# Performance work log

Measured on AMD Instinct MI355X. Metric: run time of the kernel, lower is better.

Reference implementation:

```python
import jax, jax.numpy as jnp
import numpy as np

T, N, F, H, L, E = 8, 50000, 64, 32, 64, 800000


def setup_inputs() -> dict:
    key = jax.random.key(0)
    ks = jax.random.split(key, 10)
    return {
        "x_seq": jax.random.normal(ks[0], (T, N, F), jnp.float32),
        "edge_index": jax.random.randint(ks[1], (T, 2, E), 0, N, jnp.int32),
        "conv_w": jax.random.normal(ks[2], (F, H), jnp.float32) * 0.1,
        "conv_b": jax.random.normal(ks[3], (H,), jnp.float32) * 0.1,
        "w_ih": jax.random.normal(ks[4], (4 * L, H), jnp.float32) * 0.1,
        "w_hh": jax.random.normal(ks[5], (4 * L, L), jnp.float32) * 0.1,
        "b_ih": jax.random.normal(ks[6], (4 * L,), jnp.float32) * 0.1,
        "b_hh": jax.random.normal(ks[7], (4 * L,), jnp.float32) * 0.1,
        "fc_w": jax.random.normal(ks[8], (1, L), jnp.float32) * 0.1,
        "fc_b": jax.random.normal(ks[9], (1,), jnp.float32) * 0.1,
    }


def reference(x_seq, edge_index, conv_w, conv_b, w_ih, w_hh, b_ih, b_hh, fc_w, fc_b):
    n = x_seq.shape[1]

    def gcn(x, ei):
        # GCNConv: add self loops, symmetric D^-1/2 (A+I) D^-1/2 normalization
        loop = jnp.arange(n, dtype=ei.dtype)
        src = jnp.concatenate([ei[0], loop])
        dst = jnp.concatenate([ei[1], loop])
        deg = jax.ops.segment_sum(jnp.ones_like(src, dtype=x.dtype), dst, num_segments=n)
        dinv = jnp.where(deg > 0, jax.lax.rsqrt(deg), 0.0)
        xw = x @ conv_w                              # [N,H]
        norm = dinv[src] * dinv[dst]                 # [E+N]
        msg = norm[:, None] * xw[src]                # [E+N,H]
        return jax.ops.segment_sum(msg, dst, num_segments=n) + conv_b

    h = jax.vmap(gcn)(x_seq, edge_index)             # [T,N,H]
    seq = jax.nn.relu(h).mean(axis=1)                # [T,H] mean-pool over nodes

    # single-layer LSTM, batch=1, torch gate order i,f,g,o
    l = w_hh.shape[1]

    def step(carry, xt):
        hp, cp = carry
        gates = xt @ w_ih.T + b_ih + hp @ w_hh.T + b_hh
        i, f, g, o = jnp.split(gates, 4)
        i, f, o = jax.nn.sigmoid(i), jax.nn.sigmoid(f), jax.nn.sigmoid(o)
        g = jnp.tanh(g)
        c = f * cp + i * g
        hn = o * jnp.tanh(c)
        return (hn, c), hn

    init = (jnp.zeros((l,), x_seq.dtype), jnp.zeros((l,), x_seq.dtype))
    (h_last, _), _ = jax.lax.scan(step, init, seq)
    out = h_last @ fc_w[0] + fc_b[0]                 # scalar (squeezed)
    return out
```

## Files before the change

kernel.cpp:

```cpp
#include <hip/hip_runtime.h>
#include <hip/hip_bf16.h>
#include <cstdint>
#include <cstddef>

#define T_DIM 8
#define N_NODES 50000
#define F_DIM 64
#define H_DIM 32
#define L_DIM 64
#define E_EDGES 800000

#define NB 128
#define NPB 391
#define BIN_CAP 8192
#define CHUNK_A 4000
#define DF_CAP 7400
#define NBLK_G2 782

typedef __attribute__((ext_vector_type(8))) short short8;
typedef __attribute__((ext_vector_type(4))) float f32x4;

__device__ __forceinline__ unsigned short f2bf(float f) {
  unsigned u = __float_as_uint(f);
  u = u + 0x7FFFu + ((u >> 16) & 1u);
  return (unsigned short)(u >> 16);
}
__device__ __forceinline__ float bf2f(unsigned short b) {
  return __uint_as_float(((unsigned)b) << 16);
}
__device__ __forceinline__ void addbf8(float* a, uint4 u) {
  a[0] += __uint_as_float(u.x << 16);
  a[1] += __uint_as_float(u.x & 0xFFFF0000u);
  a[2] += __uint_as_float(u.y << 16);
  a[3] += __uint_as_float(u.y & 0xFFFF0000u);
  a[4] += __uint_as_float(u.z << 16);
  a[5] += __uint_as_float(u.z & 0xFFFF0000u);
  a[6] += __uint_as_float(u.w << 16);
  a[7] += __uint_as_float(u.w & 0xFFFF0000u);
}
__device__ __forceinline__ short8 pack8(float4 lo, float4 hi) {
  short8 r;
  r[0] = (short)f2bf(lo.x); r[1] = (short)f2bf(lo.y);
  r[2] = (short)f2bf(lo.z); r[3] = (short)f2bf(lo.w);
  r[4] = (short)f2bf(hi.x); r[5] = (short)f2bf(hi.y);
  r[6] = (short)f2bf(hi.z); r[7] = (short)f2bf(hi.w);
  return r;
}

__global__ void k_part(const int* __restrict__ ei, int* __restrict__ bincur,
                       int* __restrict__ binbuf) {
  int t = blockIdx.x & 7;
  int e0 = (blockIdx.x >> 3) * CHUNK_A;
  const int4* d4 = reinterpret_cast<const int4*>(ei + (size_t)(t * 2 + 1) * E_EDGES + e0);
  const int4* s4 = reinterpret_cast<const int4*>(ei + (size_t)(t * 2 + 0) * E_EDGES + e0);
  __shared__ int hist[NB], bbase[NB], loff[NB], cur[NB];
  __shared__ unsigned sorted[CHUNK_A];
  __shared__ unsigned short dstb[CHUNK_A];
  __shared__ int wtot_sh;
  int tid = threadIdx.x;
  if (tid < NB) hist[tid] = 0;
  __syncthreads();
  for (int q = tid; q < CHUNK_A / 4; q += 256) {
    int4 d = d4[q];
    ushort4 pk;
    pk.x = (unsigned short)d.x; pk.y = (unsigned short)d.y;
    pk.z = (unsigned short)d.z; pk.w = (unsigned short)d.w;
    *reinterpret_cast<ushort4*>(&dstb[4 * q]) = pk;
    #pragma unroll
    for (int k = 0; k < 4; ++k) {
      int dst = (k == 0) ? d.x : (k == 1) ? d.y : (k == 2) ? d.z : d.w;
      atomicAdd(&hist[dst / NPB], 1);
    }
  }
  __syncthreads();
  int lane = tid & 63;
  int v = (tid < NB) ? hist[tid] : 0;
  int sc = v;
  #pragma unroll
  for (int o = 1; o < 64; o <<= 1) {
    int xx = __shfl_up(sc, o, 64);
    if (lane >= o) sc += xx;
  }
  if (tid == 63) wtot_sh = sc;
  __syncthreads();
  if (tid < NB) {
    int excl = sc - v + ((tid >= 64) ? wtot_sh : 0);
    loff[tid] = excl;
    cur[tid] = excl;
    bbase[tid] = atomicAdd(&bincur[t * NB + tid], v);
  }
  __syncthreads();
  for (int q = tid; q < CHUNK_A / 4; q += 256) {
    int4 s = s4[q];
    ushort4 dd = *reinterpret_cast<const ushort4*>(&dstb[4 * q]);
    #pragma unroll
    for (int k = 0; k < 4; ++k) {
      int dst = (k == 0) ? dd.x : (k == 1) ? dd.y : (k == 2) ? dd.z : dd.w;
      int src = (k == 0) ? s.x : (k == 1) ? s.y : (k == 2) ? s.z : s.w;
      int b = dst / NPB;
      int dl = dst - b * NPB;
      int pos = atomicAdd(&cur[b], 1);
      sorted[pos] = ((unsigned)b << 25) | ((unsigned)dl << 16) | (unsigned)src;
    }
  }
  __syncthreads();
  for (int i = tid; i < CHUNK_A; i += 256) {
    unsigned e = sorted[i];
    int b = e >> 25;
    int gpos = bbase[b] + (i - loff[b]);
    if (gpos < BIN_CAP)
      binbuf[(size_t)(t * NB + b) * BIN_CAP + gpos] = (int)(e & 0x01FFFFFFu);
  }
}

__global__ void k_degfill(const int* __restrict__ bincur, const int* __restrict__ binbuf,
                          int* __restrict__ deg, int* __restrict__ rowg,
                          unsigned short* __restrict__ colbuf) {
  int t = blockIdx.x & 7;
  int b = blockIdx.x >> 3;
  __shared__ int stage[DF_CAP];
  __shared__ unsigned short sbuf[DF_CAP];
  __shared__ int hist[NPB], rowoff[NPB + 1];
  __shared__ int wsum[4];
  int tid = threadIdx.x;
  int cnt = bincur[t * NB + b];
  if (cnt > DF_CAP) cnt = DF_CAP;
  const int* gbuf = binbuf + (size_t)(t * NB + b) * BIN_CAP;
  for (int i = tid; i < cnt; i += 256) stage[i] = gbuf[i];
  for (int i = tid; i < NPB; i += 256) hist[i] = 0;
  __syncthreads();
  for (int i = tid; i < cnt; i += 256) atomicAdd(&hist[stage[i] >> 16], 1);
  __syncthreads();
  int nb0 = b * NPB;
  for (int dl = tid; dl < NPB; dl += 256) {
    int n = nb0 + dl;
    if (n < N_NODES) deg[t * N_NODES + n] = hist[dl];
  }
  int i0 = 2 * tid, i1 = 2 * tid + 1;
  int a0 = (i0 < NPB) ? hist[i0] : 0;
  int a1 = (i1 < NPB) ? hist[i1] : 0;
  int tsum = a0 + a1;
  int lane = tid & 63, wid = tid >> 6;
  int sc = tsum;
  #pragma unroll
  for (int off = 1; off < 64; off <<= 1) {
    int o = __shfl_up(sc, off, 64);
    if (lane >= off) sc += o;
  }
  if (lane == 63) wsum[wid] = sc;
  __syncthreads();
  if (tid == 0) {
    int c = 0;
    for (int k = 0; k < 4; ++k) { int v = wsum[k]; wsum[k] = c; c += v; }
  }
  __syncthreads();
  int excl = wsum[wid] + (sc - tsum);
  if (i0 < NPB) rowoff[i0] = excl;
  if (i1 < NPB) rowoff[i1] = excl + a0;
  if (tid == 0) rowoff[NPB] = cnt;
  __syncthreads();
  int* rg = rowg + (size_t)(t * NB + b) * (NPB + 1);
  for (int i = tid; i <= NPB; i += 256) rg[i] = rowoff[i];
  for (int i = tid; i < NPB; i += 256) hist[i] = 0;
  __syncthreads();
  for (int i = tid; i < cnt; i += 256) {
    int w = stage[i];
    int dl = w >> 16;
    int pos = rowoff[dl] + atomicAdd(&hist[dl], 1);
    sbuf[pos] = (unsigned short)(w & 0xFFFF);
  }
  __syncthreads();
  unsigned short* cb = colbuf + (size_t)(t * NB + b) * BIN_CAP;
  for (int i = tid; i < cnt; i += 256) cb[i] = sbuf[i];
}

__global__ __launch_bounds__(256) void k_xw(const float* __restrict__ x,
                                            const float* __restrict__ w,
                                            const int* __restrict__ deg,
                                            unsigned short* __restrict__ s) {
  int t = blockIdx.x & 7;
  int nb = blockIdx.x >> 3;
  int wave = threadIdx.x >> 6, lane = threadIdx.x & 63;
  int node0 = nb * 64 + wave * 16;
  if (node0 >= N_NODES) return;
  int m = lane & 15, kg = lane >> 4;
  const float4* xr = reinterpret_cast<const float4*>(
      x + ((size_t)t * N_NODES + node0 + m) * F_DIM + kg * 8);
  short8 a0 = pack8(xr[0], xr[1]);
  short8 a1 = pack8(xr[8], xr[9]);
  const float* wb0 = w + (kg * 8) * H_DIM + m;
  const float* wb1 = wb0 + 32 * H_DIM;
  short8 b00, b01, b10, b11;
  #pragma unroll
  for (int j = 0; j < 8; ++j) {
    b00[j] = (short)f2bf(wb0[j * H_DIM]);
    b01[j] = (short)f2bf(wb0[j * H_DIM + 16]);
    b10[j] = (short)f2bf(wb1[j * H_DIM]);
    b11[j] = (short)f2bf(wb1[j * H_DIM + 16]);
  }
  f32x4 acc0 = {0.f, 0.f, 0.f, 0.f}, acc1 = {0.f, 0.f, 0.f, 0.f};
  acc0 = __builtin_amdgcn_mfma_f32_16x16x32_bf16(a0, b00, acc0, 0, 0, 0);
  acc0 = __builtin_amdgcn_mfma_f32_16x16x32_bf16(a1, b10, acc0, 0, 0, 0);
  acc1 = __builtin_amdgcn_mfma_f32_16x16x32_bf16(a0, b01, acc1, 0, 0, 0);
  acc1 = __builtin_amdgcn_mfma_f32_16x16x32_bf16(a1, b11, acc1, 0, 0, 0);
  unsigned short* sbase = s + ((size_t)t * N_NODES + node0) * H_DIM;
  #pragma unroll
  for (int r = 0; r < 4; ++r) {
    int row = kg * 4 + r;
    float dinv = rsqrtf((float)(deg[t * N_NODES + node0 + row] + 1));
    sbase[(size_t)row * H_DIM + m]      = f2bf(acc0[r] * dinv);
    sbase[(size_t)row * H_DIM + 16 + m] = f2bf(acc1[r] * dinv);
  }
}

__global__ void k_gather2(const unsigned short* __restrict__ s,
                          const unsigned short* __restrict__ colbuf,
                          const int* __restrict__ rowg, const float* __restrict__ conv_b,
                          float* __restrict__ partials) {
  int bid = blockIdx.x;
  int t = bid & 7;
  int gblk = bid >> 3;
  int tid = threadIdx.x;
  int g = tid >> 2, j = tid & 3;
  int n = gblk * 64 + g;
  float acc[8];
  #pragma unroll
  for (int e = 0; e < 8; ++e) acc[e] = 0.f;
  if (n < N_NODES) {
    int b = n / NPB, dl = n - b * NPB;
    const int* ro = rowg + (size_t)(t * NB + b) * (NPB + 1);
    int start = ro[dl], end = ro[dl + 1];
    float dinv = rsqrtf((float)(end - start + 1));
    const unsigned short* sbase = s + (size_t)t * N_NODES * H_DIM;
    uint4 su = *reinterpret_cast<const uint4*>(sbase + (size_t)n * H_DIM + j * 8);
    addbf8(acc, su);
    const unsigned short* col = colbuf + (size_t)(t * NB + b) * BIN_CAP;
    int p = start;
    for (; p + 4 <= end; p += 4) {
      int c0 = col[p], c1 = col[p + 1], c2 = col[p + 2], c3 = col[p + 3];
      uint4 v0 = *reinterpret_cast<const uint4*>(sbase + (size_t)c0 * H_DIM + j * 8);
      uint4 v1 = *reinterpret_cast<const uint4*>(sbase + (size_t)c1 * H_DIM + j * 8);
      uint4 v2 = *reinterpret_cast<const uint4*>(sbase + (size_t)c2 * H_DIM + j * 8);
      uint4 v3 = *reinterpret_cast<const uint4*>(sbase + (size_t)c3 * H_DIM + j * 8);
      addbf8(acc, v0);
      addbf8(acc, v1);
      addbf8(acc, v2);
      addbf8(acc, v3);
    }
    for (; p < end; ++p) {
      int c0 = col[p];
      uint4 v0 = *reinterpret_cast<const uint4*>(sbase + (size_t)c0 * H_DIM + j * 8);
      addbf8(acc, v0);
    }
    const float4* cb4 = reinterpret_cast<const float4*>(conv_b);
    float4 b0 = cb4[j * 2], b1 = cb4[j * 2 + 1];
    acc[0] = fmaxf(acc[0] * dinv + b0.x, 0.f);
    acc[1] = fmaxf(acc[1] * dinv + b0.y, 0.f);
    acc[2] = fmaxf(acc[2] * dinv + b0.z, 0.f);
    acc[3] = fmaxf(acc[3] * dinv + b0.w, 0.f);
    acc[4] = fmaxf(acc[4] * dinv + b1.x, 0.f);
    acc[5] = fmaxf(acc[5] * dinv + b1.y, 0.f);
    acc[6] = fmaxf(acc[6] * dinv + b1.z, 0.f);
    acc[7] = fmaxf(acc[7] * dinv + b1.w, 0.f);
  }
  #pragma unroll
  for (int off = 4; off < 64; off <<= 1) {
    #pragma unroll
    for (int e = 0; e < 8; ++e) acc[e] += __shfl_xor(acc[e], off, 64);
  }
  __shared__ float red[4][32];
  int wid = tid >> 6, lane = tid & 63;
  if (lane < 4) {
    #pragma unroll
    for (int e = 0; e < 8; ++e) red[wid][lane * 8 + e] = acc[e];
  }
  __syncthreads();
  if (tid < 32) {
    float sum = red[0][tid] + red[1][tid] + red[2][tid] + red[3][tid];
    partials[((size_t)t * NBLK_G2 + gblk) * H_DIM + tid] = sum;
  }
}

__global__ void k_reduce(const float* __restrict__ partials, float* __restrict__ seq_raw,
                         int nblk) {
  int t = blockIdx.x;
  int tid = threadIdx.x;
  int h = tid & 31, w = tid >> 5;
  float sum = 0.f;
  for (int b = w; b < nblk; b += 8) sum += partials[((size_t)t * nblk + b) * H_DIM + h];
  __shared__ float red[8][32];
  red[w][h] = sum;
  __syncthreads();
  if (tid < 32) {
    float sm = 0.f;
    #pragma unroll
    for (int i = 0; i < 8; ++i) sm += red[i][tid];
    seq_raw[t * H_DIM + tid] = sm;
  }
}

__global__ void k_lstm(const float* __restrict__ seq_raw, const float* __restrict__ w_ih,
                       const float* __restrict__ b_ih, const float* __restrict__ b_hh,
                       const float* __restrict__ w_hh, const float* __restrict__ fc_w,
                       const float* __restrict__ fc_b, float* __restrict__ out) {
  __shared__ float xb[T_DIM][32];
  __shared__ float gxs[T_DIM][256];
  __shared__ float hbuf[64], cbuf[64], gates[256];
  int j = threadIdx.x;
  if (j < T_DIM * 32) xb[j >> 5][j & 31] = seq_raw[j] * (1.0f / (float)N_NODES);
  if (j < 64) { hbuf[j] = 0.f; cbuf[j] = 0.f; }
  __syncthreads();
  float bsum = b_ih[j] + b_hh[j];
  for (int t = 0; t < T_DIM; ++t) {
    float gacc = bsum;
    #pragma unroll
    for (int k = 0; k < 32; ++k) gacc += w_ih[j * 32 + k] * xb[t][k];
    gxs[t][j] = gacc;
  }
  __syncthreads();
  for (int t = 0; t < T_DIM; ++t) {
    float g = gxs[t][j];
    #pragma unroll 8
    for (int k = 0; k < 64; ++k) g += w_hh[j * 64 + k] * hbuf[k];
    gates[j] = g;
    __syncthreads();
    if (j < 64) {
      float ii = 1.f / (1.f + expf(-gates[j]));
      float ff = 1.f / (1.f + expf(-gates[64 + j]));
      float gg = tanhf(gates[128 + j]);
      float oo = 1.f / (1.f + expf(-gates[192 + j]));
      float c = ff * cbuf[j] + ii * gg;
      cbuf[j] = c;
      hbuf[j] = oo * tanhf(c);
    }
    __syncthreads();
  }
  if (j == 0) {
    float acc = 0.f;
    for (int k = 0; k < 64; ++k) acc += hbuf[k] * fc_w[k];
    out[0] = acc + fc_b[0];
  }
}

extern "C" void kernel_launch(void* const* d_in, const int* in_sizes, int n_in,
                              void* d_out, int out_size, void* d_ws, size_t ws_size,
                              hipStream_t stream) {
  const float* x      = (const float*)d_in[0];
  const int*   ei     = (const int*)  d_in[1];
  const float* conv_w = (const float*)d_in[2];
  const float* conv_b = (const float*)d_in[3];
  const float* w_ih   = (const float*)d_in[4];
  const float* w_hh   = (const float*)d_in[5];
  const float* b_ih   = (const float*)d_in[6];
  const float* b_hh   = (const float*)d_in[7];
  const float* fc_w   = (const float*)d_in[8];
  const float* fc_b   = (const float*)d_in[9];
  float* out = (float*)d_out;

  char* wsb = (char*)d_ws;
  size_t off = 0;
  auto alloc = [&](size_t bytes) {
    void* p = wsb + off;
    off = (off + bytes + 255) & ~(size_t)255;
    return p;
  };
  int* bincur   = (int*)alloc(sizeof(int) * T_DIM * NB);
  int* binbuf   = (int*)alloc(sizeof(int) * (size_t)T_DIM * NB * BIN_CAP);
  unsigned short* colbuf = (unsigned short*)alloc(sizeof(unsigned short) * (size_t)T_DIM * NB * BIN_CAP);
  int* deg      = (int*)alloc(sizeof(int) * T_DIM * N_NODES);
  int* rowg     = (int*)alloc(sizeof(int) * (size_t)T_DIM * NB * (NPB + 1));
  unsigned short* s = (unsigned short*)alloc(sizeof(unsigned short) * (size_t)T_DIM * N_NODES * H_DIM);
  float* partials = (float*)alloc(sizeof(float) * (size_t)T_DIM * NBLK_G2 * H_DIM);
  float* seq_raw  = (float*)alloc(sizeof(float) * T_DIM * H_DIM);

  (void)hipMemsetAsync(bincur, 0, sizeof(int) * T_DIM * NB, stream);

  k_part<<<(E_EDGES / CHUNK_A) * T_DIM, 256, 0, stream>>>(ei, bincur, binbuf);
  k_degfill<<<NB * T_DIM, 256, 0, stream>>>(bincur, binbuf, deg, rowg, colbuf);
  k_xw<<<NBLK_G2 * T_DIM, 256, 0, stream>>>(x, conv_w, deg, s);
  k_gather2<<<NBLK_G2 * T_DIM, 256, 0, stream>>>(s, colbuf, rowg, conv_b, partials);
  k_reduce<<<T_DIM, 256, 0, stream>>>(partials, seq_raw, NBLK_G2);
  k_lstm<<<1, 256, 0, stream>>>(seq_raw, w_ih, b_ih, b_hh, w_hh, fc_w, fc_b, out);
}
```

Measured before the change: 164.6 us.

## Use dynamic per-block node scheduling in gather and stage src indices in LDS

The gather kernel now covers 256 nodes per block instead of 64. Each group of four threads grabs its next node from a shared atomic counter, which balances work across nodes with uneven degree. The ReLU outputs are accumulated per thread before the final reduction, and the neighbour loop is unrolled to 8 loads to keep more memory requests in flight. The partition kernel now loads src alongside dst in the first pass and keeps it in LDS, so the scatter pass no longer reads global memory. The tradeoffs are fewer blocks (less parallelism and tail risk), LDS atomic contention, and more register pressure.

```diff
diff --git a/kernel.cpp b/kernel.cpp
--- a/kernel.cpp
+++ b/kernel.cpp
@@ -15,7 +15,8 @@
 #define BIN_CAP 8192
 #define CHUNK_A 4000
 #define DF_CAP 7400
-#define NBLK_G2 782
+#define NPB3 256
+#define NBLK_G3 196
 
 typedef __attribute__((ext_vector_type(8))) short short8;
 typedef __attribute__((ext_vector_type(4))) float f32x4;
@@ -56,16 +57,21 @@
   __shared__ int hist[NB], bbase[NB], loff[NB], cur[NB];
   __shared__ unsigned sorted[CHUNK_A];
   __shared__ unsigned short dstb[CHUNK_A];
+  __shared__ unsigned short srcb[CHUNK_A];
   __shared__ int wtot_sh;
   int tid = threadIdx.x;
   if (tid < NB) hist[tid] = 0;
   __syncthreads();
   for (int q = tid; q < CHUNK_A / 4; q += 256) {
     int4 d = d4[q];
-    ushort4 pk;
+    int4 s = s4[q];
+    ushort4 pk, ps;
     pk.x = (unsigned short)d.x; pk.y = (unsigned short)d.y;
     pk.z = (unsigned short)d.z; pk.w = (unsigned short)d.w;
+    ps.x = (unsigned short)s.x; ps.y = (unsigned short)s.y;
+    ps.z = (unsigned short)s.z; ps.w = (unsigned short)s.w;
     *reinterpret_cast<ushort4*>(&dstb[4 * q]) = pk;
+    *reinterpret_cast<ushort4*>(&srcb[4 * q]) = ps;
     #pragma unroll
     for (int k = 0; k < 4; ++k) {
       int dst = (k == 0) ? d.x : (k == 1) ? d.y : (k == 2) ? d.z : d.w;
@@ -90,18 +96,13 @@
     bbase[tid] = atomicAdd(&bincur[t * NB + tid], v);
   }
   __syncthreads();
-  for (int q = tid; q < CHUNK_A / 4; q += 256) {
-    int4 s = s4[q];
-    ushort4 dd = *reinterpret_cast<const ushort4*>(&dstb[4 * q]);
-    #pragma unroll
-    for (int k = 0; k < 4; ++k) {
-      int dst = (k == 0) ? dd.x : (k == 1) ? dd.y : (k == 2) ? dd.z : dd.w;
-      int src = (k == 0) ? s.x : (k == 1) ? s.y : (k == 2) ? s.z : s.w;
-      int b = dst / NPB;
-      int dl = dst - b * NPB;
-      int pos = atomicAdd(&cur[b], 1);
-      sorted[pos] = ((unsigned)b << 25) | ((unsigned)dl << 16) | (unsigned)src;
-    }
+  for (int i = tid; i < CHUNK_A; i += 256) {
+    int dst = dstb[i];
+    int src = srcb[i];
+    int b = dst / NPB;
+    int dl = dst - b * NPB;
+    int pos = atomicAdd(&cur[b], 1);
+    sorted[pos] = ((unsigned)b << 25) | ((unsigned)dl << 16) | (unsigned)src;
   }
   __syncthreads();
   for (int i = tid; i < CHUNK_A; i += 256) {
@@ -213,71 +214,97 @@
   }
 }
 
-__global__ void k_gather2(const unsigned short* __restrict__ s,
+__global__ void k_gather3(const unsigned short* __restrict__ s,
                           const unsigned short* __restrict__ colbuf,
                           const int* __restrict__ rowg, const float* __restrict__ conv_b,
                           float* __restrict__ partials) {
   int bid = blockIdx.x;
   int t = bid & 7;
   int gblk = bid >> 3;
+  int base = gblk * NPB3;
   int tid = threadIdx.x;
   int g = tid >> 2, j = tid & 3;
-  int n = gblk * 64 + g;
-  float acc[8];
-  #pragma unroll
-  for (int e = 0; e < 8; ++e) acc[e] = 0.f;
-  if (n < N_NODES) {
-    int b = n / NPB, dl = n - b * NPB;
-    const int* ro = rowg + (size_t)(t * NB + b) * (NPB + 1);
-    int start = ro[dl], end = ro[dl + 1];
-    float dinv = rsqrtf((float)(end - start + 1));
-    const unsigned short* sbase = s + (size_t)t * N_NODES * H_DIM;
-    uint4 su = *reinterpret_cast<const uint4*>(sbase + (size_t)n * H_DIM + j * 8);
-    addbf8(acc, su);
-    const unsigned short* col = colbuf + (size_t)(t * NB + b) * BIN_CAP;
-    int p = start;
-    for (; p + 4 <= end; p += 4) {
-      int c0 = col[p], c1 = col[p + 1], c2 = col[p + 2], c3 = col[p + 3];
-      uint4 v0 = *reinterpret_cast<const uint4*>(sbase + (size_t)c0 * H_DIM + j * 8);
-      uint4 v1 = *reinterpret_cast<const uint4*>(sbase + (size_t)c1 * H_DIM + j * 8);
-      uint4 v2 = *reinterpret_cast<const uint4*>(sbase + (size_t)c2 * H_DIM + j * 8);
-      uint4 v3 = *reinterpret_cast<const uint4*>(sbase + (size_t)c3 * H_DIM + j * 8);
-      addbf8(acc, v0);
-      addbf8(acc, v1);
-      addbf8(acc, v2);
-      addbf8(acc, v3);
+  int lane = tid & 63;
+  __shared__ int nextn;
+  __shared__ float red[4][32];
+  if (tid == 0) nextn = 64;
+  __syncthreads();
+  const unsigned short* sbase = s + (size_t)t * N_NODES * H_DIM;
+  const float4* cb4 = reinterpret_cast<const float4*>(conv_b);
+  float4 bb0 = cb4[j * 2], bb1 = cb4[j * 2 + 1];
+  float pool[8];
+  #pragma unroll
+  for (int e = 0; e < 8; ++e) pool[e] = 0.f;
+  int idx = g;
+  while (idx < NPB3) {
+    int n = base + idx;
+    if (n < N_NODES) {
+      int b = n / NPB, dl = n - b * NPB;
+      const int* ro = rowg + (size_t)(t * NB + b) * (NPB + 1);
+      int start = ro[dl], end = ro[dl + 1];
+      float dinv = rsqrtf((float)(end - start + 1));
+      float acc[8];
+      #pragma unroll
+      for (int e = 0; e < 8; ++e) acc[e] = 0.f;
+      uint4 su = *reinterpret_cast<const uint4*>(sbase + (size_t)n * H_DIM + j * 8);
+      addbf8(acc, su);
+      const unsigned short* col = colbuf + (size_t)(t * NB + b) * BIN_CAP;
+      int p = start;
+      for (; p + 8 <= end; p += 8) {
+        int c0 = col[p], c1 = col[p + 1], c2 = col[p + 2], c3 = col[p + 3];
+        int c4 = col[p + 4], c5 = col[p + 5], c6 = col[p + 6], c7 = col[p + 7];
+        uint4 v0 = *reinterpret_cast<const uint4*>(sbase + (size_t)c0 * H_DIM + j * 8);
+        uint4 v1 = *reinterpret_cast<const uint4*>(sbase + (size_t)c1 * H_DIM + j * 8);
+        uint4 v2 = *reinterpret_cast<const uint4*>(sbase + (size_t)c2 * H_DIM + j * 8);
+        uint4 v3 = *reinterpret_cast<const uint4*>(sbase + (size_t)c3 * H_DIM + j * 8);
+        uint4 v4 = *reinterpret_cast<const uint4*>(sbase + (size_t)c4 * H_DIM + j * 8);
+        uint4 v5 = *reinterpret_cast<const uint4*>(sbase + (size_t)c5 * H_DIM + j * 8);
+        uint4 v6 = *reinterpret_cast<const uint4*>(sbase + (size_t)c6 * H_DIM + j * 8);
+        uint4 v7 = *reinterpret_cast<const uint4*>(sbase + (size_t)c7 * H_DIM + j * 8);
+        addbf8(acc, v0); addbf8(acc, v1); addbf8(acc, v2); addbf8(acc, v3);
+        addbf8(acc, v4); addbf8(acc, v5); addbf8(acc, v6); addbf8(acc, v7);
+      }
+      for (; p + 4 <= end; p += 4) {
+        int c0 = col[p], c1 = col[p + 1], c2 = col[p + 2], c3 = col[p + 3];
+        uint4 v0 = *reinterpret_cast<const uint4*>(sbase + (size_t)c0 * H_DIM + j * 8);
+        uint4 v1 = *reinterpret_cast<const uint4*>(sbase + (size_t)c1 * H_DIM + j * 8);
+        uint4 v2 = *reinterpret_cast<const uint4*>(sbase + (size_t)c2 * H_DIM + j * 8);
+        uint4 v3 = *reinterpret_cast<const uint4*>(sbase + (size_t)c3 * H_DIM + j * 8);
+        addbf8(acc, v0); addbf8(acc, v1); addbf8(acc, v2); addbf8(acc, v3);
+      }
+      for (; p < end; ++p) {
+        int c0 = col[p];
+        uint4 v0 = *reinterpret_cast<const uint4*>(sbase + (size_t)c0 * H_DIM + j * 8);
+        addbf8(acc, v0);
+      }
+      pool[0] += fmaxf(acc[0] * dinv + bb0.x, 0.f);
+      pool[1] += fmaxf(acc[1] * dinv + bb0.y, 0.f);
+      pool[2] += fmaxf(acc[2] * dinv + bb0.z, 0.f);
+      pool[3] += fmaxf(acc[3] * dinv + bb0.w, 0.f);
+      pool[4] += fmaxf(acc[4] * dinv + bb1.x, 0.f);
+      pool[5] += fmaxf(acc[5] * dinv + bb1.y, 0.f);
+      pool[6] += fmaxf(acc[6] * dinv + bb1.z, 0.f);
+      pool[7] += fmaxf(acc[7] * dinv + bb1.w, 0.f);
     }
-    for (; p < end; ++p) {
-      int c0 = col[p];
-      uint4 v0 = *reinterpret_cast<const uint4*>(sbase + (size_t)c0 * H_DIM + j * 8);
-      addbf8(acc, v0);
-    }
-    const float4* cb4 = reinterpret_cast<const float4*>(conv_b);
-    float4 b0 = cb4[j * 2], b1 = cb4[j * 2 + 1];
-    acc[0] = fmaxf(acc[0] * dinv + b0.x, 0.f);
-    acc[1] = fmaxf(acc[1] * dinv + b0.y, 0.f);
-    acc[2] = fmaxf(acc[2] * dinv + b0.z, 0.f);
-    acc[3] = fmaxf(acc[3] * dinv + b0.w, 0.f);
-    acc[4] = fmaxf(acc[4] * dinv + b1.x, 0.f);
-    acc[5] = fmaxf(acc[5] * dinv + b1.y, 0.f);
-    acc[6] = fmaxf(acc[6] * dinv + b1.z, 0.f);
-    acc[7] = fmaxf(acc[7] * dinv + b1.w, 0.f);
+    int nn = 0;
+    if ((lane & 3) == 0) nn = atomicAdd(&nextn, 1);
+    nn = __shfl(nn, lane & 60, 64);
+    idx = nn;
   }
   #pragma unroll
   for (int off = 4; off < 64; off <<= 1) {
     #pragma unroll
-    for (int e = 0; e < 8; ++e) acc[e] += __shfl_xor(acc[e], off, 64);
-  }
-  __shared__ float red[4][32];
-  int wid = tid >> 6, lane = tid & 63;
+    for (int e = 0; e < 8; ++e) pool[e] += __shfl_xor(pool[e], off, 64);
+  }
+  int wid = tid >> 6;
   if (lane < 4) {
     #pragma unroll
-    for (int e = 0; e < 8; ++e) red[wid][lane * 8 + e] = acc[e];
+    for (int e = 0; e < 8; ++e) red[wid][lane * 8 + e] = pool[e];
   }
   __syncthreads();
   if (tid < 32) {
     float sum = red[0][tid] + red[1][tid] + red[2][tid] + red[3][tid];
-    partials[((size_t)t * NBLK_G2 + gblk) * H_DIM + tid] = sum;
+    partials[((size_t)t * NBLK_G3 + gblk) * H_DIM + tid] = sum;
   }
 }
 
@@ -370,15 +397,15 @@
   int* deg      = (int*)alloc(sizeof(int) * T_DIM * N_NODES);
   int* rowg     = (int*)alloc(sizeof(int) * (size_t)T_DIM * NB * (NPB + 1));
   unsigned short* s = (unsigned short*)alloc(sizeof(unsigned short) * (size_t)T_DIM * N_NODES * H_DIM);
-  float* partials = (float*)alloc(sizeof(float) * (size_t)T_DIM * NBLK_G2 * H_DIM);
+  float* partials = (float*)alloc(sizeof(float) * (size_t)T_DIM * NBLK_G3 * H_DIM);
   float* seq_raw  = (float*)alloc(sizeof(float) * T_DIM * H_DIM);
 
   (void)hipMemsetAsync(bincur, 0, sizeof(int) * T_DIM * NB, stream);
 
   k_part<<<(E_EDGES / CHUNK_A) * T_DIM, 256, 0, stream>>>(ei, bincur, binbuf);
   k_degfill<<<NB * T_DIM, 256, 0, stream>>>(bincur, binbuf, deg, rowg, colbuf);
-  k_xw<<<NBLK_G2 * T_DIM, 256, 0, stream>>>(x, conv_w, deg, s);
-  k_gather2<<<NBLK_G2 * T_DIM, 256, 0, stream>>>(s, colbuf, rowg, conv_b, partials);
-  k_reduce<<<T_DIM, 256, 0, stream>>>(partials, seq_raw, NBLK_G2);
+  k_xw<<<782 * T_DIM, 256, 0, stream>>>(x, conv_w, deg, s);
+  k_gather3<<<NBLK_G3 * T_DIM, 256, 0, stream>>>(s, colbuf, rowg, conv_b, partials);
+  k_reduce<<<T_DIM, 256, 0, stream>>>(partials, seq_raw, NBLK_G3);
   k_lstm<<<1, 256, 0, stream>>>(seq_raw, w_ih, b_ih, b_hh, w_hh, fc_w, fc_b, out);
 }
```

Result: faster. 154.9 us (-5.8%).
